# Kernel tuning notes

Measured on AMD Instinct MI355X. Metric: run time of the kernel, lower is better.

The kernel has to match this reference:

```python
import jax, jax.numpy as jnp
import numpy as np

B, T, D_MODEL = 2, 2048, 2048
NH, NKV, DH = 16, 4, 128
N_REP = NH // NKV
NV = 256  # n_vision_tokens
THETA = 10000.0
NEG = -1e9


def setup_inputs() -> dict:
    key = jax.random.key(0)
    ks = jax.random.split(key, 5)
    x = jax.random.normal(ks[0], (B, T, D_MODEL), jnp.float32)
    # rope_freqs = exp(i * t * theta^{-2j/D}) represented as cos/sin, shape [T, DH//2]
    inv = 1.0 / (THETA ** (np.arange(0, DH, 2, dtype=np.float64) / DH))
    ang = np.outer(np.arange(T, dtype=np.float64), inv)
    cos = jnp.asarray(np.cos(ang), jnp.float32)
    sin = jnp.asarray(np.sin(ang), jnp.float32)
    sc = 0.02
    wq = jax.random.normal(ks[1], (D_MODEL, NH * DH), jnp.float32) * sc
    wk = jax.random.normal(ks[2], (D_MODEL, NKV * DH), jnp.float32) * sc
    wv = jax.random.normal(ks[3], (D_MODEL, NKV * DH), jnp.float32) * sc
    wo = jax.random.normal(ks[4], (NH * DH, D_MODEL), jnp.float32) * sc
    return {"x": x, "cos": cos, "sin": sin, "wq": wq, "wk": wk, "wv": wv,
            "wo": wo, "n_vision_tokens": NV}


def _rope(t, cos, sin):
    # t: [B,H,L,D]; pairs (even=real, odd=imag); cos/sin: [L, D//2]
    a = t[..., 0::2]
    b = t[..., 1::2]
    c = cos[None, None]
    s = sin[None, None]
    ra = a * c - b * s
    rb = a * s + b * c
    return jnp.stack([ra, rb], axis=-1).reshape(t.shape)


def reference(x, cos, sin, wq, wk, wv, wo, n_vision_tokens):
    Bx, Tx, _ = x.shape
    nv = int(n_vision_tokens)
    tl = Tx - nv  # text length

    q = (x @ wq).reshape(Bx, Tx, NH, DH).transpose(0, 2, 1, 3)   # [B,NH,T,DH]
    k = (x @ wk).reshape(Bx, Tx, NKV, DH).transpose(0, 2, 1, 3)  # [B,NKV,T,DH]
    v = (x @ wv).reshape(Bx, Tx, NKV, DH).transpose(0, 2, 1, 3)

    # RoPE only on the text portion (vision tokens keep raw q/k)
    c, s = cos[:tl], sin[:tl]
    q = jnp.concatenate([q[:, :, :nv], _rope(q[:, :, nv:], c, s)], axis=2)
    k = jnp.concatenate([k[:, :, :nv], _rope(k[:, :, nv:], c, s)], axis=2)

    new_kv_cache = (k, v)

    # GQA: repeat_interleave KV heads
    k = jnp.repeat(k, N_REP, axis=1)
    v = jnp.repeat(v, N_REP, axis=1)

    attn = jnp.einsum('bhqd,bhkd->bhqk', q, k) / jnp.sqrt(jnp.float32(DH))

    # hybrid mask: vision rows/cols fully visible; text-text strictly causal
    text_mask = jnp.triu(jnp.ones((tl, tl), bool), k=1)
    mask = jnp.zeros((Tx, Tx), bool).at[nv:, nv:].set(text_mask)
    attn = jnp.where(mask[None, None], NEG, attn)

    attn = jax.nn.softmax(attn, axis=-1)
    out = jnp.einsum('bhqk,bhkd->bhqd', attn, v)
    out = out.transpose(0, 2, 1, 3).reshape(Bx, Tx, NH * DH) @ wo
    return out, new_kv_cache
```

## Files before the change

kernel.cpp:

```cpp
#include <hip/hip_runtime.h>
#include <hip/hip_bf16.h>

#define BB 2
#define TT 2048
#define DMODEL 2048
#define NH 16
#define NKV 4
#define DH 128
#define NV 256
#define TL (TT - NV)
#define NQKV 3072

typedef __bf16  bf16x8  __attribute__((ext_vector_type(8)));
typedef float   float4v __attribute__((ext_vector_type(4)));
typedef short   short8  __attribute__((ext_vector_type(8)));
typedef unsigned short ushort;

__device__ __forceinline__ float bf2f(ushort u) {
    union { float f; unsigned i; } c; c.i = ((unsigned)u) << 16; return c.f;
}
__device__ __forceinline__ ushort f2bf(float f) {
    union { float f; unsigned i; } c; c.f = f;
    unsigned r = c.i + 0x7fff + ((c.i >> 16) & 1);
    return (ushort)(r >> 16);
}

#define GLDS16(g, l) __builtin_amdgcn_global_load_lds( \
    (__attribute__((address_space(1))) void*)(g), \
    (__attribute__((address_space(3))) void*)(l), 16, 0, 0)

__global__ __launch_bounds__(256) void convert_x(
    const float* __restrict__ x, ushort* __restrict__ xbf)
{
    size_t i = ((size_t)blockIdx.x * 256 + threadIdx.x) * 8;
    float4v f0 = *(const float4v*)&x[i];
    float4v f1 = *(const float4v*)&x[i + 4];
    short8 h;
    h[0] = (short)f2bf(f0[0]); h[1] = (short)f2bf(f0[1]);
    h[2] = (short)f2bf(f0[2]); h[3] = (short)f2bf(f0[3]);
    h[4] = (short)f2bf(f1[0]); h[5] = (short)f2bf(f1[1]);
    h[6] = (short)f2bf(f1[2]); h[7] = (short)f2bf(f1[3]);
    *(short8*)&xbf[i] = h;
}

__global__ __launch_bounds__(256) void wtrans(
    const float* __restrict__ w, ushort* __restrict__ wT, int K, int N)
{
    __shared__ ushort st[64][72];
    int n0 = blockIdx.x * 64, k0 = blockIdx.y * 64;
    int r  = threadIdx.x >> 2;
    int c0 = (threadIdx.x & 3) * 16;
    #pragma unroll
    for (int j = 0; j < 16; j += 4) {
        float4v f = *(const float4v*)&w[(size_t)(k0 + r) * N + n0 + c0 + j];
        st[c0 + j + 0][r] = f2bf(f[0]);
        st[c0 + j + 1][r] = f2bf(f[1]);
        st[c0 + j + 2][r] = f2bf(f[2]);
        st[c0 + j + 3][r] = f2bf(f[3]);
    }
    __syncthreads();
    ushort* dst = &wT[(size_t)(n0 + r) * K + k0];
    *(short8*)&dst[c0]     = *(short8*)&st[r][c0];
    *(short8*)&dst[c0 + 8] = *(short8*)&st[r][c0 + 8];
}

__global__ __launch_bounds__(256) void wtrans_wo(
    const float* __restrict__ w, ushort* __restrict__ qkv)
{
    __shared__ ushort st[64][72];
    int n0 = blockIdx.x * 64, k0 = blockIdx.y * 64;
    int r  = threadIdx.x >> 2;
    int c0 = (threadIdx.x & 3) * 16;
    #pragma unroll
    for (int j = 0; j < 16; j += 4) {
        float4v f = *(const float4v*)&w[(size_t)(k0 + r) * DMODEL + n0 + c0 + j];
        st[c0 + j + 0][r] = f2bf(f[0]);
        st[c0 + j + 1][r] = f2bf(f[1]);
        st[c0 + j + 2][r] = f2bf(f[2]);
        st[c0 + j + 3][r] = f2bf(f[3]);
    }
    __syncthreads();
    ushort* dst = qkv + ((size_t)(2 * (n0 + r) + (k0 >> 10))) * NQKV + 2048 + (k0 & 1023);
    *(short8*)&dst[c0]     = *(short8*)&st[r][c0];
    *(short8*)&dst[c0 + 8] = *(short8*)&st[r][c0 + 8];
}

__global__ __launch_bounds__(256) void vtrans(
    const ushort* __restrict__ qkv, ushort* __restrict__ vbfT)
{
    __shared__ ushort st[64][72];
    int t0 = blockIdx.x * 64, d0 = blockIdx.y * 64;
    int bk = blockIdx.z;
    int b = bk >> 2, kh = bk & 3;
    int r  = threadIdx.x >> 2;
    int c0 = (threadIdx.x & 3) * 16;
    const ushort* src = qkv + ((size_t)(b * TT + t0 + r)) * NQKV + 2560 + kh * DH + d0;
    short8 a0 = *(const short8*)&src[c0];
    short8 a1 = *(const short8*)&src[c0 + 8];
    #pragma unroll
    for (int j = 0; j < 8; j++) {
        st[c0 + j][r]     = (ushort)a0[j];
        st[c0 + 8 + j][r] = (ushort)a1[j];
    }
    __syncthreads();
    ushort* dst = vbfT + ((size_t)(bk * DH + d0 + r)) * TT + t0;
    *(short8*)&dst[c0]     = *(short8*)&st[r][c0];
    *(short8*)&dst[c0 + 8] = *(short8*)&st[r][c0 + 8];
}

__global__ __launch_bounds__(256) void gemm_lds(
    const ushort* __restrict__ A, int lda,
    const ushort* __restrict__ BT,
    ushort* __restrict__ C, int ldc, int K)
{
    __shared__ ushort As[128 * 32];
    __shared__ ushort Bs[128 * 32];

    int tid = threadIdx.x;
    int wave = tid >> 6, lane = tid & 63, quad = lane >> 4, l16 = lane & 15;
    int m0 = blockIdx.y * 128, n0 = blockIdx.x * 128;
    int wr = (wave >> 1) * 64, wc = (wave & 1) * 64;

    int srow = tid >> 2, scol = (tid & 3) * 8;
    const ushort* ag = A  + (size_t)(m0 + srow) * lda + scol;
    const ushort* bg = BT + (size_t)(n0 + srow) * K   + scol;
    ushort* la0 = As + (wave * 16) * 32;
    ushort* la1 = As + (64 + wave * 16) * 32;
    ushort* lb0 = Bs + (wave * 16) * 32;
    ushort* lb1 = Bs + (64 + wave * 16) * 32;

    float4v acc[4][4];
    for (int i = 0; i < 4; i++)
        for (int j = 0; j < 4; j++)
            acc[i][j] = (float4v){0.f, 0.f, 0.f, 0.f};

    for (int k0 = 0; k0 < K; k0 += 32) {
        GLDS16(ag + k0,                     la0);
        GLDS16(ag + (size_t)64 * lda + k0,  la1);
        GLDS16(bg + k0,                     lb0);
        GLDS16(bg + (size_t)64 * K + k0,    lb1);
        __syncthreads();

        bf16x8 af[4], bfr[4];
        #pragma unroll
        for (int i = 0; i < 4; i++) af[i] = *(const bf16x8*)&As[(wr + i * 16 + l16) * 32 + quad * 8];
        #pragma unroll
        for (int j = 0; j < 4; j++) bfr[j] = *(const bf16x8*)&Bs[(wc + j * 16 + l16) * 32 + quad * 8];
        #pragma unroll
        for (int i = 0; i < 4; i++)
            #pragma unroll
            for (int j = 0; j < 4; j++)
                acc[i][j] = __builtin_amdgcn_mfma_f32_16x16x32_bf16(af[i], bfr[j], acc[i][j], 0, 0, 0);
        __syncthreads();
    }

    #pragma unroll
    for (int i = 0; i < 4; i++)
        #pragma unroll
        for (int j = 0; j < 4; j++)
            #pragma unroll
            for (int r = 0; r < 4; r++) {
                int row = m0 + wr + i * 16 + quad * 4 + r;
                int col = n0 + wc + j * 16 + l16;
                C[(size_t)row * ldc + col] = f2bf(acc[i][j][r]);
            }
}

__global__ __launch_bounds__(256) void gemm_out(
    const ushort* __restrict__ A,
    const ushort* __restrict__ Bc,
    float* __restrict__ C)
{
    __shared__ ushort As[128 * 32];
    __shared__ ushort Bs[128 * 32];

    int tid = threadIdx.x;
    int wave = tid >> 6, lane = tid & 63, quad = lane >> 4, l16 = lane & 15;
    int m0 = blockIdx.y * 128, n0 = blockIdx.x * 128;
    int wr = (wave >> 1) * 64, wc = (wave & 1) * 64;

    int srow = tid >> 2, scol = (tid & 3) * 8;
    const ushort* ag = A  + (size_t)(m0 + srow) * NQKV + scol;
    const ushort* bg = Bc + (size_t)(n0 + srow) * 6144 + scol;
    ushort* la0 = As + (wave * 16) * 32;
    ushort* la1 = As + (64 + wave * 16) * 32;
    ushort* lb0 = Bs + (wave * 16) * 32;
    ushort* lb1 = Bs + (64 + wave * 16) * 32;

    float4v acc[4][4];
    for (int i = 0; i < 4; i++)
        for (int j = 0; j < 4; j++)
            acc[i][j] = (float4v){0.f, 0.f, 0.f, 0.f};

    for (int k0 = 0; k0 < 2048; k0 += 32) {
        int koff = ((k0 >> 10) * NQKV) + (k0 & 1023);
        GLDS16(ag + k0,                       la0);
        GLDS16(ag + (size_t)64 * NQKV + k0,   la1);
        GLDS16(bg + koff,                     lb0);
        GLDS16(bg + (size_t)64 * 6144 + koff, lb1);
        __syncthreads();

        bf16x8 af[4], bfr[4];
        #pragma unroll
        for (int i = 0; i < 4; i++) af[i] = *(const bf16x8*)&As[(wr + i * 16 + l16) * 32 + quad * 8];
        #pragma unroll
        for (int j = 0; j < 4; j++) bfr[j] = *(const bf16x8*)&Bs[(wc + j * 16 + l16) * 32 + quad * 8];
        #pragma unroll
        for (int i = 0; i < 4; i++)
            #pragma unroll
            for (int j = 0; j < 4; j++)
                acc[i][j] = __builtin_amdgcn_mfma_f32_16x16x32_bf16(af[i], bfr[j], acc[i][j], 0, 0, 0);
        __syncthreads();
    }

    #pragma unroll
    for (int i = 0; i < 4; i++)
        #pragma unroll
        for (int j = 0; j < 4; j++)
            #pragma unroll
            for (int r = 0; r < 4; r++) {
                int row = m0 + wr + i * 16 + quad * 4 + r;
                int col = n0 + wc + j * 16 + l16;
                C[(size_t)row * DMODEL + col] = acc[i][j][r];
            }
}

__global__ __launch_bounds__(256) void rope_q(
    ushort* __restrict__ qkv, const float* __restrict__ cosp, const float* __restrict__ sinp)
{
    int idx = blockIdx.x * 256 + threadIdx.x;
    int b = blockIdx.y;
    int i  = idx & 63;
    int h  = (idx >> 6) & 15;
    int tr = idx >> 10;
    int t  = NV + tr;
    size_t off = ((size_t)(b * TT + t)) * NQKV + h * DH + 2 * i;
    unsigned pk = *(const unsigned*)&qkv[off];
    float a  = bf2f((ushort)(pk & 0xffff));
    float bb = bf2f((ushort)(pk >> 16));
    float c  = cosp[tr * 64 + i];
    float s  = sinp[tr * 64 + i];
    *(unsigned*)&qkv[off] = (unsigned)f2bf(a * c - bb * s) | ((unsigned)f2bf(a * s + bb * c) << 16);
}

__global__ __launch_bounds__(256) void ropek_cache(
    const ushort* __restrict__ qkv,
    const float* __restrict__ cosp, const float* __restrict__ sinp,
    float* __restrict__ kout, float* __restrict__ vout, ushort* __restrict__ kbf)
{
    int idx = blockIdx.x * 256 + threadIdx.x;
    int i  = idx & 63;
    int kh = (idx >> 6) & 3;
    int t  = (idx >> 8) & 2047;
    int b  = idx >> 19;
    size_t row = ((size_t)(b * TT + t)) * NQKV;
    size_t dst = ((size_t)((b * NKV + kh) * TT + t)) * DH + 2 * i;
    unsigned pk = *(const unsigned*)&qkv[row + 2048 + kh * DH + 2 * i];
    float ka = bf2f((ushort)(pk & 0xffff));
    float kb = bf2f((ushort)(pk >> 16));
    if (t >= NV) {
        int pos = t - NV;
        float c = cosp[pos * 64 + i];
        float s = sinp[pos * 64 + i];
        float ra = ka * c - kb * s;
        float rb = ka * s + kb * c;
        ka = ra; kb = rb;
    }
    kout[dst]     = ka;
    kout[dst + 1] = kb;
    *(unsigned*)&kbf[dst] = (unsigned)f2bf(ka) | ((unsigned)f2bf(kb) << 16);
    unsigned pv = *(const unsigned*)&qkv[row + 2560 + kh * DH + 2 * i];
    vout[dst]     = bf2f((ushort)(pv & 0xffff));
    vout[dst + 1] = bf2f((ushort)(pv >> 16));
}

__global__ __launch_bounds__(256, 2) void attn_kernel(
    ushort* qkv,
    const ushort* __restrict__ kbf, const ushort* __restrict__ vbfT)
{
    __shared__ ushort shm[32768];

    int tid = threadIdx.x;
    int wave = tid >> 6, lane = tid & 63, quad = lane >> 4, l16 = lane & 15;
    int qx = blockIdx.x;
    int qt = (qx < 4) ? qx : (35 - qx);
    int h = blockIdx.y, b = blockIdx.z;
    int kh = h >> 2;
    int q0 = qt * 64;

    int srow = tid >> 2, scol = (tid & 3) * 8;

    ushort* qbase = qkv + ((size_t)(b * TT) + q0) * NQKV + h * DH;
    #pragma unroll
    for (int dk = 0; dk < 4; dk++)
        GLDS16(qbase + (size_t)srow * NQKV + dk * 32 + scol, shm + dk * 2048 + wave * 512);
    __syncthreads();
    bf16x8 qf[4];
    #pragma unroll
    for (int dk = 0; dk < 4; dk++)
        qf[dk] = *(const bf16x8*)&shm[dk * 2048 + (wave * 16 + l16) * 32 + quad * 8];
    __syncthreads();

    float4v Oacc[8];
    #pragma unroll
    for (int i = 0; i < 8; i++) Oacc[i] = (float4v){0.f, 0.f, 0.f, 0.f};
    float mrow = -1e30f, lrow = 0.f;

    int nkt = (q0 < NV) ? (TT / 64) : (qt + 1);
    const float scale = 0.08838834764831845f;
    int qg = q0 + wave * 16 + l16;

    const ushort* kb2 = kbf  + ((size_t)(b * NKV + kh)) * TT * DH;
    const ushort* vb2 = vbfT + ((size_t)(b * NKV + kh)) * DH * TT;

    int sl0 = ((lane & 16) << 1) + l16;
    int sl1 = sl0 + 16;
    bool hi = lane >= 32;

    auto stage = [&](int buf, int kt) {
        ushort* Kb = shm + buf * 16384;
        ushort* Vb = Kb + 8192;
        int k0 = kt * 64;
        #pragma unroll
        for (int dk = 0; dk < 4; dk++)
            GLDS16(kb2 + (size_t)(k0 + srow) * DH + dk * 32 + scol, Kb + dk * 2048 + wave * 512);
        #pragma unroll
        for (int kk = 0; kk < 2; kk++)
            #pragma unroll
            for (int p = 0; p < 2; p++)
                GLDS16(vb2 + (size_t)(p * 64 + srow) * TT + k0 + kk * 32 + scol,
                       Vb + kk * 4096 + (p * 64 + wave * 16) * 32);
    };

    stage(0, 0);

    for (int kt = 0; kt < nkt; kt++) {
        int cur = kt & 1;
        __syncthreads();
        if (kt + 1 < nkt)
            stage(cur ^ 1, kt + 1);

        const ushort* Kc = shm + cur * 16384;
        const ushort* Vc = Kc + 8192;
        int k0 = kt * 64;

        float4v sacc[4];
        #pragma unroll
        for (int t2i = 0; t2i < 4; t2i++) {
            float4v a4 = (float4v){0.f, 0.f, 0.f, 0.f};
            #pragma unroll
            for (int dk = 0; dk < 4; dk++) {
                bf16x8 af = *(const bf16x8*)&Kc[dk * 2048 + (t2i * 16 + l16) * 32 + quad * 8];
                a4 = __builtin_amdgcn_mfma_f32_16x16x32_bf16(af, qf[dk], a4, 0, 0, 0);
            }
            sacc[t2i] = a4;
        }

        bool diag = (q0 >= NV) && (kt == qt);
        #pragma unroll
        for (int t2i = 0; t2i < 4; t2i++)
            #pragma unroll
            for (int i = 0; i < 4; i++) {
                float s = sacc[t2i][i] * scale;
                if (diag && (k0 + t2i * 16 + quad * 4 + i > qg)) s = -1e9f;
                sacc[t2i][i] = s;
            }

        float mx = -1e30f;
        #pragma unroll
        for (int t2i = 0; t2i < 4; t2i++)
            #pragma unroll
            for (int i = 0; i < 4; i++) mx = fmaxf(mx, sacc[t2i][i]);
        mx = fmaxf(mx, __shfl_xor(mx, 16, 64));
        mx = fmaxf(mx, __shfl_xor(mx, 32, 64));
        float mnew = fmaxf(mrow, mx);
        float alpha = __expf(mrow - mnew);
        float ss = 0.f;
        #pragma unroll
        for (int t2i = 0; t2i < 4; t2i++)
            #pragma unroll
            for (int i = 0; i < 4; i++) {
                float p = __expf(sacc[t2i][i] - mnew);
                sacc[t2i][i] = p;
                ss += p;
            }
        ss += __shfl_xor(ss, 16, 64);
        ss += __shfl_xor(ss, 32, 64);
        lrow = lrow * alpha + ss;
        mrow = mnew;
        #pragma unroll
        for (int dt = 0; dt < 8; dt++)
            #pragma unroll
            for (int i = 0; i < 4; i++) Oacc[dt][i] *= alpha;

        unsigned p01[4], p23[4];
        #pragma unroll
        for (int t2i = 0; t2i < 4; t2i++) {
            p01[t2i] = (unsigned)f2bf(sacc[t2i][0]) | ((unsigned)f2bf(sacc[t2i][1]) << 16);
            p23[t2i] = (unsigned)f2bf(sacc[t2i][2]) | ((unsigned)f2bf(sacc[t2i][3]) << 16);
        }

        #pragma unroll
        for (int kk = 0; kk < 2; kk++) {
            int ta = 2 * kk, tb = 2 * kk + 1;
            unsigned A0 = __shfl(p01[ta], sl0, 64), B0 = __shfl(p01[tb], sl0, 64);
            unsigned A1 = __shfl(p23[ta], sl0, 64), B1 = __shfl(p23[tb], sl0, 64);
            unsigned A2 = __shfl(p01[ta], sl1, 64), B2 = __shfl(p01[tb], sl1, 64);
            unsigned A3 = __shfl(p23[ta], sl1, 64), B3 = __shfl(p23[tb], sl1, 64);
            union { unsigned u[4]; bf16x8 v; } pf;
            pf.u[0] = hi ? B0 : A0;
            pf.u[1] = hi ? B1 : A1;
            pf.u[2] = hi ? B2 : A2;
            pf.u[3] = hi ? B3 : A3;
            #pragma unroll
            for (int dt = 0; dt < 8; dt++) {
                bf16x8 vf = *(const bf16x8*)&Vc[kk * 4096 + (dt * 16 + l16) * 32 + quad * 8];
                Oacc[dt] = __builtin_amdgcn_mfma_f32_16x16x32_bf16(vf, pf.v, Oacc[dt], 0, 0, 0);
            }
        }
    }

    float rinv = 1.f / lrow;
    size_t orow = (size_t)(wave * 16 + l16) * NQKV;
    #pragma unroll
    for (int dt = 0; dt < 8; dt++)
        #pragma unroll
        for (int i = 0; i < 4; i += 2) {
            unsigned pk = (unsigned)f2bf(Oacc[dt][i] * rinv)
                        | ((unsigned)f2bf(Oacc[dt][i + 1] * rinv) << 16);
            *(unsigned*)&qbase[orow + dt * 16 + quad * 4 + i] = pk;
        }
}

extern "C" void kernel_launch(void* const* d_in, const int* in_sizes, int n_in,
                              void* d_out, int out_size, void* d_ws, size_t ws_size,
                              hipStream_t stream) {
    const float* x    = (const float*)d_in[0];
    const float* cosp = (const float*)d_in[1];
    const float* sinp = (const float*)d_in[2];
    const float* wq   = (const float*)d_in[3];
    const float* wk   = (const float*)d_in[4];
    const float* wv   = (const float*)d_in[5];
    const float* wo   = (const float*)d_in[6];

    float* out  = (float*)d_out;
    float* kout = out + (size_t)BB * TT * DMODEL;
    float* vout = kout + (size_t)BB * NKV * TT * DH;

    ushort* sc    = (ushort*)d_out;
    ushort* wqkvT = sc;
    ushort* xbf   = sc + (size_t)NQKV * DMODEL;
    ushort* kbf   = sc + (size_t)NQKV * DMODEL;
    ushort* vbfT  = kbf + (size_t)BB * NKV * TT * DH;

    ushort* qkv = (ushort*)d_ws;

    const int M = BB * TT;

    convert_x<<<dim3((size_t)M * DMODEL / 2048), 256, 0, stream>>>(x, xbf);
    wtrans<<<dim3(DMODEL / 64, DMODEL / 64), 256, 0, stream>>>(wq, wqkvT, DMODEL, DMODEL);
    wtrans<<<dim3((NKV * DH) / 64, DMODEL / 64), 256, 0, stream>>>(wk, wqkvT + (size_t)2048 * DMODEL, DMODEL, NKV * DH);
    wtrans<<<dim3((NKV * DH) / 64, DMODEL / 64), 256, 0, stream>>>(wv, wqkvT + (size_t)2560 * DMODEL, DMODEL, NKV * DH);

    gemm_lds<<<dim3(NQKV / 128, M / 128), 256, 0, stream>>>(
        xbf, DMODEL, wqkvT, qkv, NQKV, DMODEL);

    rope_q<<<dim3(TL * NH * 64 / 256, BB), 256, 0, stream>>>(qkv, cosp, sinp);
    ropek_cache<<<dim3((BB * TT * NKV * 64) / 256), 256, 0, stream>>>(qkv, cosp, sinp, kout, vout, kbf);
    vtrans<<<dim3(TT / 64, DH / 64, BB * NKV), 256, 0, stream>>>(qkv, vbfT);

    wtrans_wo<<<dim3(DMODEL / 64, DMODEL / 64), 256, 0, stream>>>(wo, qkv);

    attn_kernel<<<dim3(TT / 64, NH, BB), 256, 0, stream>>>(qkv, kbf, vbfT);

    gemm_out<<<dim3(DMODEL / 128, M / 128), 256, 0, stream>>>(qkv, qkv + 2048, out);
}
```

Measured before the change: 420.7 us.

## Process two query heads per attention block to reuse K/V tiles

Each attention block now handles two query heads that share the same KV head. Every K/V tile staged into shared memory therefore feeds two sets of MFMAs, and the grid shrinks by half along the head dimension. This halves K/V global-to-LDS traffic per unit of work. In exchange, accumulator and Q-fragment registers double, which may spill or cut occupancy under the 256x2 launch bounds, and there are fewer blocks to balance the causal workload.

Result: faster. 386.1 us (-8.2%).

```diff
diff --git a/kernel.cpp b/kernel.cpp
--- a/kernel.cpp
+++ b/kernel.cpp
@@ -284,27 +284,37 @@
     int wave = tid >> 6, lane = tid & 63, quad = lane >> 4, l16 = lane & 15;
     int qx = blockIdx.x;
     int qt = (qx < 4) ? qx : (35 - qx);
-    int h = blockIdx.y, b = blockIdx.z;
-    int kh = h >> 2;
+    int hy = blockIdx.y, b = blockIdx.z;
+    int h0 = hy * 2;
+    int kh = hy >> 1;
     int q0 = qt * 64;
 
     int srow = tid >> 2, scol = (tid & 3) * 8;
 
-    ushort* qbase = qkv + ((size_t)(b * TT) + q0) * NQKV + h * DH;
-    #pragma unroll
-    for (int dk = 0; dk < 4; dk++)
-        GLDS16(qbase + (size_t)srow * NQKV + dk * 32 + scol, shm + dk * 2048 + wave * 512);
+    ushort* qbase0 = qkv + ((size_t)(b * TT) + q0) * NQKV + h0 * DH;
+    ushort* qbase1 = qbase0 + DH;
+    #pragma unroll
+    for (int dk = 0; dk < 4; dk++) {
+        GLDS16(qbase0 + (size_t)srow * NQKV + dk * 32 + scol, shm + dk * 2048 + wave * 512);
+        GLDS16(qbase1 + (size_t)srow * NQKV + dk * 32 + scol, shm + 16384 + dk * 2048 + wave * 512);
+    }
     __syncthreads();
-    bf16x8 qf[4];
-    #pragma unroll
-    for (int dk = 0; dk < 4; dk++)
-        qf[dk] = *(const bf16x8*)&shm[dk * 2048 + (wave * 16 + l16) * 32 + quad * 8];
+    bf16x8 qf0[4], qf1[4];
+    #pragma unroll
+    for (int dk = 0; dk < 4; dk++) {
+        qf0[dk] = *(const bf16x8*)&shm[dk * 2048 + (wave * 16 + l16) * 32 + quad * 8];
+        qf1[dk] = *(const bf16x8*)&shm[16384 + dk * 2048 + (wave * 16 + l16) * 32 + quad * 8];
+    }
     __syncthreads();
 
-    float4v Oacc[8];
-    #pragma unroll
-    for (int i = 0; i < 8; i++) Oacc[i] = (float4v){0.f, 0.f, 0.f, 0.f};
-    float mrow = -1e30f, lrow = 0.f;
+    float4v O0[8], O1[8];
+    #pragma unroll
+    for (int i = 0; i < 8; i++) {
+        O0[i] = (float4v){0.f, 0.f, 0.f, 0.f};
+        O1[i] = (float4v){0.f, 0.f, 0.f, 0.f};
+    }
+    float m0r = -1e30f, l0r = 0.f;
+    float m1r = -1e30f, l1r = 0.f;
 
     int nkt = (q0 < NV) ? (TT / 64) : (qt + 1);
     const float scale = 0.08838834764831845f;
@@ -344,16 +354,18 @@
         const ushort* Vc = Kc + 8192;
         int k0 = kt * 64;
 
-        float4v sacc[4];
+        float4v s0[4], s1[4];
         #pragma unroll
         for (int t2i = 0; t2i < 4; t2i++) {
-            float4v a4 = (float4v){0.f, 0.f, 0.f, 0.f};
+            float4v a0 = (float4v){0.f, 0.f, 0.f, 0.f};
+            float4v a1 = (float4v){0.f, 0.f, 0.f, 0.f};
             #pragma unroll
             for (int dk = 0; dk < 4; dk++) {
                 bf16x8 af = *(const bf16x8*)&Kc[dk * 2048 + (t2i * 16 + l16) * 32 + quad * 8];
-                a4 = __builtin_amdgcn_mfma_f32_16x16x32_bf16(af, qf[dk], a4, 0, 0, 0);
-            }
-            sacc[t2i] = a4;
+                a0 = __builtin_amdgcn_mfma_f32_16x16x32_bf16(af, qf0[dk], a0, 0, 0, 0);
+                a1 = __builtin_amdgcn_mfma_f32_16x16x32_bf16(af, qf1[dk], a1, 0, 0, 0);
+            }
+            s0[t2i] = a0; s1[t2i] = a1;
         }
 
         bool diag = (q0 >= NV) && (kt == qt);
@@ -361,74 +373,99 @@
         for (int t2i = 0; t2i < 4; t2i++)
             #pragma unroll
             for (int i = 0; i < 4; i++) {
-                float s = sacc[t2i][i] * scale;
-                if (diag && (k0 + t2i * 16 + quad * 4 + i > qg)) s = -1e9f;
-                sacc[t2i][i] = s;
-            }
-
-        float mx = -1e30f;
+                bool msk = diag && (k0 + t2i * 16 + quad * 4 + i > qg);
+                float v0 = s0[t2i][i] * scale; if (msk) v0 = -1e9f; s0[t2i][i] = v0;
+                float v1 = s1[t2i][i] * scale; if (msk) v1 = -1e9f; s1[t2i][i] = v1;
+            }
+
+        float mx0 = -1e30f, mx1 = -1e30f;
         #pragma unroll
         for (int t2i = 0; t2i < 4; t2i++)
             #pragma unroll
-            for (int i = 0; i < 4; i++) mx = fmaxf(mx, sacc[t2i][i]);
-        mx = fmaxf(mx, __shfl_xor(mx, 16, 64));
-        mx = fmaxf(mx, __shfl_xor(mx, 32, 64));
-        float mnew = fmaxf(mrow, mx);
-        float alpha = __expf(mrow - mnew);
-        float ss = 0.f;
+            for (int i = 0; i < 4; i++) {
+                mx0 = fmaxf(mx0, s0[t2i][i]);
+                mx1 = fmaxf(mx1, s1[t2i][i]);
+            }
+        mx0 = fmaxf(mx0, __shfl_xor(mx0, 16, 64));
+        mx0 = fmaxf(mx0, __shfl_xor(mx0, 32, 64));
+        mx1 = fmaxf(mx1, __shfl_xor(mx1, 16, 64));
+        mx1 = fmaxf(mx1, __shfl_xor(mx1, 32, 64));
+        float mn0 = fmaxf(m0r, mx0), mn1 = fmaxf(m1r, mx1);
+        float al0 = __expf(m0r - mn0), al1 = __expf(m1r - mn1);
+        float ss0 = 0.f, ss1 = 0.f;
         #pragma unroll
         for (int t2i = 0; t2i < 4; t2i++)
             #pragma unroll
             for (int i = 0; i < 4; i++) {
-                float p = __expf(sacc[t2i][i] - mnew);
-                sacc[t2i][i] = p;
-                ss += p;
-            }
-        ss += __shfl_xor(ss, 16, 64);
-        ss += __shfl_xor(ss, 32, 64);
-        lrow = lrow * alpha + ss;
-        mrow = mnew;
+                float p0 = __expf(s0[t2i][i] - mn0); s0[t2i][i] = p0; ss0 += p0;
+                float p1 = __expf(s1[t2i][i] - mn1); s1[t2i][i] = p1; ss1 += p1;
+            }
+        ss0 += __shfl_xor(ss0, 16, 64); ss0 += __shfl_xor(ss0, 32, 64);
+        ss1 += __shfl_xor(ss1, 16, 64); ss1 += __shfl_xor(ss1, 32, 64);
+        l0r = l0r * al0 + ss0; m0r = mn0;
+        l1r = l1r * al1 + ss1; m1r = mn1;
         #pragma unroll
         for (int dt = 0; dt < 8; dt++)
             #pragma unroll
-            for (int i = 0; i < 4; i++) Oacc[dt][i] *= alpha;
-
-        unsigned p01[4], p23[4];
+            for (int i = 0; i < 4; i++) {
+                O0[dt][i] *= al0;
+                O1[dt][i] *= al1;
+            }
+
+        unsigned p01a[4], p23a[4], p01b[4], p23b[4];
         #pragma unroll
         for (int t2i = 0; t2i < 4; t2i++) {
-            p01[t2i] = (unsigned)f2bf(sacc[t2i][0]) | ((unsigned)f2bf(sacc[t2i][1]) << 16);
-            p23[t2i] = (unsigned)f2bf(sacc[t2i][2]) | ((unsigned)f2bf(sacc[t2i][3]) << 16);
+            p01a[t2i] = (unsigned)f2bf(s0[t2i][0]) | ((unsigned)f2bf(s0[t2i][1]) << 16);
+            p23a[t2i] = (unsigned)f2bf(s0[t2i][2]) | ((unsigned)f2bf(s0[t2i][3]) << 16);
+            p01b[t2i] = (unsigned)f2bf(s1[t2i][0]) | ((unsigned)f2bf(s1[t2i][1]) << 16);
+            p23b[t2i] = (unsigned)f2bf(s1[t2i][2]) | ((unsigned)f2bf(s1[t2i][3]) << 16);
         }
 
         #pragma unroll
         for (int kk = 0; kk < 2; kk++) {
             int ta = 2 * kk, tb = 2 * kk + 1;
-            unsigned A0 = __shfl(p01[ta], sl0, 64), B0 = __shfl(p01[tb], sl0, 64);
-            unsigned A1 = __shfl(p23[ta], sl0, 64), B1 = __shfl(p23[tb], sl0, 64);
-            unsigned A2 = __shfl(p01[ta], sl1, 64), B2 = __shfl(p01[tb], sl1, 64);
-            unsigned A3 = __shfl(p23[ta], sl1, 64), B3 = __shfl(p23[tb], sl1, 64);
-            union { unsigned u[4]; bf16x8 v; } pf;
-            pf.u[0] = hi ? B0 : A0;
-            pf.u[1] = hi ? B1 : A1;
-            pf.u[2] = hi ? B2 : A2;
-            pf.u[3] = hi ? B3 : A3;
+            union { unsigned u[4]; bf16x8 v; } pf0, pf1;
+            {
+                unsigned A0 = __shfl(p01a[ta], sl0, 64), B0 = __shfl(p01a[tb], sl0, 64);
+                unsigned A1 = __shfl(p23a[ta], sl0, 64), B1 = __shfl(p23a[tb], sl0, 64);
+                unsigned A2 = __shfl(p01a[ta], sl1, 64), B2 = __shfl(p01a[tb], sl1, 64);
+                unsigned A3 = __shfl(p23a[ta], sl1, 64), B3 = __shfl(p23a[tb], sl1, 64);
+                pf0.u[0] = hi ? B0 : A0;
+                pf0.u[1] = hi ? B1 : A1;
+                pf0.u[2] = hi ? B2 : A2;
+                pf0.u[3] = hi ? B3 : A3;
+            }
+            {
+                unsigned A0 = __shfl(p01b[ta], sl0, 64), B0 = __shfl(p01b[tb], sl0, 64);
+                unsigned A1 = __shfl(p23b[ta], sl0, 64), B1 = __shfl(p23b[tb], sl0, 64);
+                unsigned A2 = __shfl(p01b[ta], sl1, 64), B2 = __shfl(p01b[tb], sl1, 64);
+                unsigned A3 = __shfl(p23b[ta], sl1, 64), B3 = __shfl(p23b[tb], sl1, 64);
+                pf1.u[0] = hi ? B0 : A0;
+                pf1.u[1] = hi ? B1 : A1;
+                pf1.u[2] = hi ? B2 : A2;
+                pf1.u[3] = hi ? B3 : A3;
+            }
             #pragma unroll
             for (int dt = 0; dt < 8; dt++) {
                 bf16x8 vf = *(const bf16x8*)&Vc[kk * 4096 + (dt * 16 + l16) * 32 + quad * 8];
-                Oacc[dt] = __builtin_amdgcn_mfma_f32_16x16x32_bf16(vf, pf.v, Oacc[dt], 0, 0, 0);
+                O0[dt] = __builtin_amdgcn_mfma_f32_16x16x32_bf16(vf, pf0.v, O0[dt], 0, 0, 0);
+                O1[dt] = __builtin_amdgcn_mfma_f32_16x16x32_bf16(vf, pf1.v, O1[dt], 0, 0, 0);
             }
         }
     }
 
-    float rinv = 1.f / lrow;
+    float rinv0 = 1.f / l0r, rinv1 = 1.f / l1r;
     size_t orow = (size_t)(wave * 16 + l16) * NQKV;
     #pragma unroll
     for (int dt = 0; dt < 8; dt++)
         #pragma unroll
         for (int i = 0; i < 4; i += 2) {
-            unsigned pk = (unsigned)f2bf(Oacc[dt][i] * rinv)
-                        | ((unsigned)f2bf(Oacc[dt][i + 1] * rinv) << 16);
-            *(unsigned*)&qbase[orow + dt * 16 + quad * 4 + i] = pk;
+            unsigned pk0 = (unsigned)f2bf(O0[dt][i] * rinv0)
+                         | ((unsigned)f2bf(O0[dt][i + 1] * rinv0) << 16);
+            unsigned pk1 = (unsigned)f2bf(O1[dt][i] * rinv1)
+                         | ((unsigned)f2bf(O1[dt][i + 1] * rinv1) << 16);
+            *(unsigned*)&qbase0[orow + dt * 16 + quad * 4 + i] = pk0;
+            *(unsigned*)&qbase1[orow + dt * 16 + quad * 4 + i] = pk1;
         }
 }
 
@@ -471,7 +508,7 @@
 
     wtrans_wo<<<dim3(DMODEL / 64, DMODEL / 64), 256, 0, stream>>>(wo, qkv);
 
-    attn_kernel<<<dim3(TT / 64, NH, BB), 256, 0, stream>>>(qkv, kbf, vbfT);
+    attn_kernel<<<dim3(TT / 64, NH / 2, BB), 256, 0, stream>>>(qkv, kbf, vbfT);
 
     gemm_out<<<dim3(DMODEL / 128, M / 128), 256, 0, stream>>>(qkv, qkv + 2048, out);
 }
```
